# Kernel tuning notes

Hardware: AMD Instinct MI355X
Metric: run time of the kernel (lower is better)

Reference implementation:

```python
import jax, jax.numpy as jnp
import numpy as np

GRID_SIZE = 128
FEATURE_SIZE = 16
HIDDEN_SIZE = 64
N_POINTS = 2097152


def setup_inputs() -> dict:
    key = jax.random.key(0)
    ks = jax.random.split(key, 8)
    points = jax.random.uniform(ks[0], (N_POINTS, 3), dtype=jnp.float32)
    grid = jax.random.normal(ks[1], (GRID_SIZE, GRID_SIZE, GRID_SIZE, FEATURE_SIZE), dtype=jnp.float32)
    # torch nn.Linear default init: U(-1/sqrt(fan_in), 1/sqrt(fan_in))
    def linear(k, fan_in, fan_out):
        kw, kb = jax.random.split(k)
        bound = 1.0 / np.sqrt(fan_in)
        W = jax.random.uniform(kw, (fan_out, fan_in), minval=-bound, maxval=bound, dtype=jnp.float32)
        b = jax.random.uniform(kb, (fan_out,), minval=-bound, maxval=bound, dtype=jnp.float32)
        return W, b
    W1, b1 = linear(ks[2], FEATURE_SIZE, HIDDEN_SIZE)
    W2, b2 = linear(ks[3], HIDDEN_SIZE, HIDDEN_SIZE)
    W3, b3 = linear(ks[4], HIDDEN_SIZE, 1)
    return {"points": points, "grid": grid, "W1": W1, "b1": b1,
            "W2": W2, "b2": b2, "W3": W3, "b3": b3}


def reference(points, grid, W1, b1, W2, b2, W3, b3):
    gs = grid.shape[0]
    # nearest-grid-node index: scale to [0, gs-1], clamp, round
    p = jnp.clip(points * (gs - 1), 0.0, gs - 1)
    idx = jnp.round(p).astype(jnp.int32)  # (N, 3)
    feats = grid[idx[:, 0], idx[:, 1], idx[:, 2]]  # (N, F) gather
    h = jax.nn.relu(feats @ W1.T + b1)
    h = jax.nn.relu(h @ W2.T + b2)
    occ = jnp.tanh(h @ W3.T + b3)  # (N, 1)
    return occ
```

## Files before the change

kernel.cpp:

```cpp
#include <hip/hip_runtime.h>
#include <hip/hip_fp16.h>
#include <cstdint>
#include <cstddef>


typedef _Float16 half8 __attribute__((ext_vector_type(8)));
typedef float float4v __attribute__((ext_vector_type(4)));

#define WPB 4
#define NT  16
#define NP  8

__device__ inline uint32_t pack_f16x2(float a, float b) {
    union { _Float16 h[2]; uint32_t u; } v;
    v.h[0] = (_Float16)a;
    v.h[1] = (_Float16)b;
    return v.u;
}

__global__ __launch_bounds__(256, 3) void occ_mlp_kernel(
    const float* __restrict__ pts,
    const float* __restrict__ grid,
    const float* __restrict__ W1, const float* __restrict__ b1,
    const float* __restrict__ W2, const float* __restrict__ b2,
    const float* __restrict__ W3, const float* __restrict__ b3,
    float* __restrict__ out, int nPoints)
{
    const int lane = threadIdx.x & 63;
    const int l15  = lane & 15;
    const int quad = lane >> 4;
    const int wib  = threadIdx.x >> 6;
    const int tile0 = (blockIdx.x * WPB + wib) * NT;
    const int nTiles = (nPoints + 15) >> 4;
    if (tile0 >= nTiles) return;
    const int maxP = nPoints - 1;
    const int pt0  = tile0 << 4;

    const int half = quad & 1;
    const int tsel = quad >> 1;

    half8 A1[4];
#pragma unroll
    for (int t = 0; t < 4; ++t) {
        half8 f = {};
        if (quad < 2) {
            const float* row = W1 + (16 * t + l15) * 16 + quad * 8;
#pragma unroll
            for (int j = 0; j < 8; ++j) f[j] = (_Float16)row[j];
        } else if (quad == 2) {
            f[0] = (_Float16)b1[16 * t + l15];
        }
        A1[t] = f;
    }
    half8 A2[4][2];
#pragma unroll
    for (int t = 0; t < 4; ++t)
#pragma unroll
        for (int kk = 0; kk < 2; ++kk) {
            const float* row = W2 + (16 * t + l15) * 64 + 32 * kk + 8 * quad;
            half8 f;
#pragma unroll
            for (int j = 0; j < 8; ++j) f[j] = (_Float16)row[j];
            A2[t][kk] = f;
        }
    float4v bias2[4];
    float w3v[4][4];
#pragma unroll
    for (int t = 0; t < 4; ++t)
#pragma unroll
        for (int r = 0; r < 4; ++r) {
            int h = 16 * t + 4 * quad + r;
            bias2[t][r] = b2[h];
            w3v[t][r]   = W3[h];
        }
    const float bias3 = b3[0];

    const int src0 = l15 + 16 * ((2 * quad) & 3);
    const int src1 = l15 + 16 * ((2 * quad + 1) & 3);
    const bool sel = (quad >> 1) != 0;

    float Cx[3], Cy[3], Cz[3];
    float4 Fa[4], Fb[4];

    auto loadCoords = [&](int slot, int v) {
        int p = pt0 + v * 32 + (tsel << 4) + l15;
        p = p > maxP ? maxP : p;
        const float* q = pts + 3 * p;
        Cx[slot] = q[0]; Cy[slot] = q[1]; Cz[slot] = q[2];
    };
    auto loadFeat = [&](int fslot, int cslot) {
        const int ix = (int)rintf(fminf(fmaxf(Cx[cslot] * 127.0f, 0.0f), 127.0f));
        const int iy = (int)rintf(fminf(fmaxf(Cy[cslot] * 127.0f, 0.0f), 127.0f));
        const int iz = (int)rintf(fminf(fmaxf(Cz[cslot] * 127.0f, 0.0f), 127.0f));
        const int ofs = ((((ix << 7) | iy) << 7) | iz) << 4;
        const float4* g = reinterpret_cast<const float4*>(grid + ofs + (half << 3));
        Fa[fslot] = g[0];
        Fb[fslot] = g[1];
    };

    loadCoords(0, 0); loadCoords(1, 1); loadCoords(2, 2);
    loadFeat(0, 0); loadFeat(1, 1); loadFeat(2, 2);
    loadCoords(0, 3); loadCoords(1, 4);

    float o[4];

#pragma unroll
    for (int v = 0; v < NP; ++v) {
        const int s = v & 3;

#pragma unroll
        for (int tt = 0; tt < 2; ++tt) {
            const int u = 2 * v + tt;

            float4 f0, f1;
            if (tt == 0) {
                f0 = Fa[s];
                f1 = Fb[s];
            } else {
                f0.x = __shfl_xor(Fa[s].x, 32); f0.y = __shfl_xor(Fa[s].y, 32);
                f0.z = __shfl_xor(Fa[s].z, 32); f0.w = __shfl_xor(Fa[s].w, 32);
                f1.x = __shfl_xor(Fb[s].x, 32); f1.y = __shfl_xor(Fb[s].y, 32);
                f1.z = __shfl_xor(Fb[s].z, 32); f1.w = __shfl_xor(Fb[s].w, 32);
            }

            half8 bfrag = {};
            if (quad < 2) {
                bfrag[0] = (_Float16)f0.x; bfrag[1] = (_Float16)f0.y;
                bfrag[2] = (_Float16)f0.z; bfrag[3] = (_Float16)f0.w;
                bfrag[4] = (_Float16)f1.x; bfrag[5] = (_Float16)f1.y;
                bfrag[6] = (_Float16)f1.z; bfrag[7] = (_Float16)f1.w;
            } else if (quad == 2) {
                bfrag[0] = (_Float16)1.0f;
            }

            if (tt == 0) {
                if (v + 3 < NP) loadFeat((v + 3) & 3, v % 3);
                if (v + 5 < NP) loadCoords((v + 2) % 3, v + 5);
            }

            float4v C1[4];
#pragma unroll
            for (int t = 0; t < 4; ++t) {
                float4v zacc = {};
                C1[t] = __builtin_amdgcn_mfma_f32_16x16x32_f16(A1[t], bfrag, zacc, 0, 0, 0);
            }

            uint32_t P[4][2];
#pragma unroll
            for (int t = 0; t < 4; ++t) {
                P[t][0] = pack_f16x2(fmaxf(C1[t][0], 0.0f), fmaxf(C1[t][1], 0.0f));
                P[t][1] = pack_f16x2(fmaxf(C1[t][2], 0.0f), fmaxf(C1[t][3], 0.0f));
            }

            union Frag { uint32_t u[4]; half8 h; } B2[2];
#pragma unroll
            for (int kk = 0; kk < 2; ++kk) {
                const uint32_t x0a = (uint32_t)__shfl((int)P[2 * kk    ][0], src0);
                const uint32_t x0b = (uint32_t)__shfl((int)P[2 * kk + 1][0], src0);
                const uint32_t x1a = (uint32_t)__shfl((int)P[2 * kk    ][1], src0);
                const uint32_t x1b = (uint32_t)__shfl((int)P[2 * kk + 1][1], src0);
                const uint32_t y0a = (uint32_t)__shfl((int)P[2 * kk    ][0], src1);
                const uint32_t y0b = (uint32_t)__shfl((int)P[2 * kk + 1][0], src1);
                const uint32_t y1a = (uint32_t)__shfl((int)P[2 * kk    ][1], src1);
                const uint32_t y1b = (uint32_t)__shfl((int)P[2 * kk + 1][1], src1);
                B2[kk].u[0] = sel ? x0b : x0a;
                B2[kk].u[1] = sel ? x1b : x1a;
                B2[kk].u[2] = sel ? y0b : y0a;
                B2[kk].u[3] = sel ? y1b : y1a;
            }

            float4v C2[4];
#pragma unroll
            for (int t = 0; t < 4; ++t) C2[t] = bias2[t];
#pragma unroll
            for (int kk = 0; kk < 2; ++kk)
#pragma unroll
                for (int t = 0; t < 4; ++t)
                    C2[t] = __builtin_amdgcn_mfma_f32_16x16x32_f16(A2[t][kk], B2[kk].h, C2[t], 0, 0, 0);

            float z = 0.0f;
#pragma unroll
            for (int t = 0; t < 4; ++t)
#pragma unroll
                for (int r = 0; r < 4; ++r)
                    z = fmaf(fmaxf(C2[t][r], 0.0f), w3v[t][r], z);
            z += __shfl_xor(z, 16);
            z += __shfl_xor(z, 32);
            const float e = __expf(2.0f * (z + bias3));
            o[u & 3] = fmaf(-2.0f, __builtin_amdgcn_rcpf(e + 1.0f), 1.0f);

            if ((u & 3) == 3) {
                const float osel = (quad == 0) ? o[0] : (quad == 1) ? o[1]
                                 : (quad == 2) ? o[2] : o[3];
                const int pstore = (tile0 + (u & ~3)) * 16 + lane;
                if (pstore <= maxP) out[pstore] = osel;
            }
        }

        asm volatile("" ::: "memory");
    }
}

extern "C" void kernel_launch(void* const* d_in, const int* in_sizes, int n_in,
                              void* d_out, int out_size, void* d_ws, size_t ws_size,
                              hipStream_t stream)
{
    const float* pts  = (const float*)d_in[0];
    const float* grid = (const float*)d_in[1];
    const float* W1   = (const float*)d_in[2];
    const float* b1   = (const float*)d_in[3];
    const float* W2   = (const float*)d_in[4];
    const float* b2   = (const float*)d_in[5];
    const float* W3   = (const float*)d_in[6];
    const float* b3   = (const float*)d_in[7];
    float* out = (float*)d_out;
    const int nPoints = in_sizes[0] / 3;

    const int nTiles = (nPoints + 15) >> 4;
    const int tilesPerBlock = WPB * NT;
    const int nBlocks = (nTiles + tilesPerBlock - 1) / tilesPerBlock;

    occ_mlp_kernel<<<dim3(nBlocks), dim3(256), 0, stream>>>(
        pts, grid, W1, b1, W2, b2, W3, b3, out, nPoints);
}
```

Measured before the change: 249.7 us.

## Deepen gather prefetch to five slots and use packed-fp16 ReLU conversion

```diff
diff --git a/kernel.cpp b/kernel.cpp
--- a/kernel.cpp
+++ b/kernel.cpp
@@ -5,17 +5,20 @@
 
 
 typedef _Float16 half8 __attribute__((ext_vector_type(8)));
+typedef __fp16  fp16v2 __attribute__((ext_vector_type(2)));
 typedef float float4v __attribute__((ext_vector_type(4)));
 
 #define WPB 4
 #define NT  16
 #define NP  8
-
-__device__ inline uint32_t pack_f16x2(float a, float b) {
-    union { _Float16 h[2]; uint32_t u; } v;
-    v.h[0] = (_Float16)a;
-    v.h[1] = (_Float16)b;
-    return v.u;
+#define FD  5
+
+__device__ inline uint32_t relu_pk(float a, float b) {
+    union { fp16v2 h; uint32_t u; } c;
+    fp16v2 h = __builtin_amdgcn_cvt_pkrtz(a, b);
+    fp16v2 z = {};
+    c.h = __builtin_elementwise_max(h, z);
+    return c.u;
 }
 
 __global__ __launch_bounds__(256, 3) void occ_mlp_kernel(
@@ -80,7 +83,7 @@
     const bool sel = (quad >> 1) != 0;
 
     float Cx[3], Cy[3], Cz[3];
-    float4 Fa[4], Fb[4];
+    float4 Fa[FD], Fb[FD];
 
     auto loadCoords = [&](int slot, int v) {
         int p = pt0 + v * 32 + (tsel << 4) + l15;
@@ -101,27 +104,31 @@
     loadCoords(0, 0); loadCoords(1, 1); loadCoords(2, 2);
     loadFeat(0, 0); loadFeat(1, 1); loadFeat(2, 2);
     loadCoords(0, 3); loadCoords(1, 4);
+    loadFeat(3, 0); loadFeat(4, 1);
+    loadCoords(2, 5); loadCoords(0, 6);
 
     float o[4];
 
 #pragma unroll
     for (int v = 0; v < NP; ++v) {
-        const int s = v & 3;
+        const int s = v % FD;
+
+        const float4 a0 = Fa[s];
+        const float4 a1 = Fb[s];
+        float4 b0, b1v;
+        b0.x  = __shfl_xor(Fa[s].x, 32); b0.y  = __shfl_xor(Fa[s].y, 32);
+        b0.z  = __shfl_xor(Fa[s].z, 32); b0.w  = __shfl_xor(Fa[s].w, 32);
+        b1v.x = __shfl_xor(Fb[s].x, 32); b1v.y = __shfl_xor(Fb[s].y, 32);
+        b1v.z = __shfl_xor(Fb[s].z, 32); b1v.w = __shfl_xor(Fb[s].w, 32);
+
+        if (v + FD < NP) loadFeat(s, (v + FD) % 3);
+        if (v + 7  < NP) loadCoords((v + 7) % 3, v + 7);
 
 #pragma unroll
         for (int tt = 0; tt < 2; ++tt) {
             const int u = 2 * v + tt;
-
-            float4 f0, f1;
-            if (tt == 0) {
-                f0 = Fa[s];
-                f1 = Fb[s];
-            } else {
-                f0.x = __shfl_xor(Fa[s].x, 32); f0.y = __shfl_xor(Fa[s].y, 32);
-                f0.z = __shfl_xor(Fa[s].z, 32); f0.w = __shfl_xor(Fa[s].w, 32);
-                f1.x = __shfl_xor(Fb[s].x, 32); f1.y = __shfl_xor(Fb[s].y, 32);
-                f1.z = __shfl_xor(Fb[s].z, 32); f1.w = __shfl_xor(Fb[s].w, 32);
-            }
+            const float4 f0 = tt ? b0 : a0;
+            const float4 f1 = tt ? b1v : a1;
 
             half8 bfrag = {};
             if (quad < 2) {
@@ -133,11 +140,6 @@
                 bfrag[0] = (_Float16)1.0f;
             }
 
-            if (tt == 0) {
-                if (v + 3 < NP) loadFeat((v + 3) & 3, v % 3);
-                if (v + 5 < NP) loadCoords((v + 2) % 3, v + 5);
-            }
-
             float4v C1[4];
 #pragma unroll
             for (int t = 0; t < 4; ++t) {
@@ -148,8 +150,8 @@
             uint32_t P[4][2];
 #pragma unroll
             for (int t = 0; t < 4; ++t) {
-                P[t][0] = pack_f16x2(fmaxf(C1[t][0], 0.0f), fmaxf(C1[t][1], 0.0f));
-                P[t][1] = pack_f16x2(fmaxf(C1[t][2], 0.0f), fmaxf(C1[t][3], 0.0f));
+                P[t][0] = relu_pk(C1[t][0], C1[t][1]);
+                P[t][1] = relu_pk(C1[t][2], C1[t][3]);
             }
 
             union Frag { uint32_t u[4]; half8 h; } B2[2];
```

Measured after the change: 274.4 us. 9.9% more time.
